# Performance work log

Hardware: AMD Instinct MI355X
Metric: run time of the kernel (lower is better)

## Reference

```python
import jax, jax.numpy as jnp
import numpy as np

CHEB_K = 2  # hops per support; stacked terms = 1 + 2*CHEB_K = 5


def setup_inputs() -> dict:
    key = jax.random.key(0)
    k1, k2, k3, k4, k5 = jax.random.split(key, 5)
    B, N, C, O, D = 16, 1024, 64, 64, 10
    return {
        "x": jax.random.normal(k1, (B, N, C), dtype=jnp.float32),
        "adj": jax.random.uniform(k2, (2, B, N, N), dtype=jnp.float32),
        "node_embedding": jax.random.normal(k3, (N, D), dtype=jnp.float32),
        "weights_pool": jax.random.normal(k4, (D, 2 * CHEB_K + 1, C, O), dtype=jnp.float32) * 0.1,
        "bias_pool": jax.random.normal(k5, (D, O), dtype=jnp.float32) * 0.1,
    }


def reference(x, adj, node_embedding, weights_pool, bias_pool):
    # k-hop graph aggregation over each of the 2 supports
    out = [x]
    for s in range(adj.shape[0]):
        a = adj[s]  # [B, N, N]
        x1 = x
        for _ in range(CHEB_K):
            x1 = jnp.einsum('bnm,bmc->bnc', a, x1)
            out.append(x1)
    x_g = jnp.stack(out, axis=2)  # [B, N, K, C] with K = 2*cheb_k+1 (already node-major)
    # per-node hypernetwork weights and bias from node embeddings
    weights = jnp.einsum('nd,dkio->nkio', node_embedding, weights_pool)  # [N, K, C, O]
    bias = node_embedding @ bias_pool  # [N, O]
    # per-node contraction over (K, C)
    return jnp.einsum('bnki,nkio->bno', x_g, weights) + bias
```

## Files before the change

### kernel.cpp

```cpp
#include <hip/hip_runtime.h>
#include <stdint.h>


typedef __attribute__((ext_vector_type(4))) float f32x4;
typedef __attribute__((ext_vector_type(2))) float f32x2;
typedef __attribute__((ext_vector_type(8))) short s16x8;
typedef __attribute__((ext_vector_type(8))) __bf16 bf16x8;

__device__ __forceinline__ unsigned short f2bf(float f) {
  union { float f; uint32_t u; } v; v.f = f;
  uint32_t r = v.u + 0x7FFFu + ((v.u >> 16) & 1u);
  return (unsigned short)(r >> 16);
}
__device__ __forceinline__ uint32_t pack2(float a, float b) {
  return (uint32_t)f2bf(a) | ((uint32_t)f2bf(b) << 16);
}

union FragU { s16x8 s; bf16x8 b; };

__device__ __forceinline__ void async_cp16(const void* g, void* l) {
  __builtin_amdgcn_global_load_lds(
      (const __attribute__((address_space(1))) void*)g,
      (__attribute__((address_space(3))) void*)l, 16, 0, 0);
}

#define WAITVM(n)                                                         \
  __builtin_amdgcn_s_waitcnt(((n) & 15) | ((((n) >> 4) & 3) << 14) |      \
                             (7 << 4) | (15 << 8))

__global__ __launch_bounds__(256) void prep(const float* __restrict__ x,
                                            const float* __restrict__ wp,
                                            unsigned short* __restrict__ XT0,
                                            float* __restrict__ wpT) {
  __shared__ __align__(16) char smem[17160];
  const int tid = threadIdx.x;
  const int bid = blockIdx.x;
  if (bid < 256) {
    unsigned short (*tl)[72] = (unsigned short(*)[72])smem;
    const int b = bid >> 4, n0 = (bid & 15) * 64;
    {
      const int c4 = (tid & 15) * 4;
#pragma unroll
      for (int i = 0; i < 4; ++i) {
        const int row = (tid >> 4) + i * 16;
        f32x4 v =
            *(const f32x4*)(x + ((size_t)(b * 1024 + n0 + row)) * 64 + c4);
        *(uint32_t*)&tl[row][c4]     = pack2(v[0], v[1]);
        *(uint32_t*)&tl[row][c4 + 2] = pack2(v[2], v[3]);
      }
    }
    __syncthreads();
    {
      const int c = tid >> 2;
      const int nch = (tid & 3) * 16;
      s16x8 s0, s1;
#pragma unroll
      for (int j = 0; j < 8; ++j) {
        s0[j] = (short)tl[nch + j][c];
        s1[j] = (short)tl[nch + 8 + j][c];
      }
      unsigned short* p = XT0 + (size_t)(b * 64 + c) * 1024 + n0 + nch;
      *(s16x8*)p = s0;
      *(s16x8*)(p + 8) = s1;
    }
  } else {
    float (*tl)[65] = (float(*)[65])smem;
    const int jj = bid - 256;
    const int d = jj / 5, ki0 = (jj % 5) * 64;
    const float* src = wp + (size_t)d * 20480;
    {
      const int o4 = (tid & 15) * 4;
#pragma unroll
      for (int i = 0; i < 4; ++i) {
        const int row = (tid >> 4) + i * 16;
        f32x4 v = *(const f32x4*)(src + (size_t)(ki0 + row) * 64 + o4);
        tl[row][o4] = v[0]; tl[row][o4 + 1] = v[1];
        tl[row][o4 + 2] = v[2]; tl[row][o4 + 3] = v[3];
      }
    }
    __syncthreads();
    {
      const int o = tid >> 2;
      const int kch = (tid & 3) * 16;
      float* dst = wpT + (size_t)d * 20480 + (size_t)o * 320 + ki0 + kch;
#pragma unroll
      for (int u = 0; u < 4; ++u) {
        f32x4 v = { tl[kch + 4 * u][o], tl[kch + 4 * u + 1][o],
                    tl[kch + 4 * u + 2][o], tl[kch + 4 * u + 3][o] };
        *(f32x4*)(dst + 4 * u) = v;
      }
    }
  }
}

__device__ __forceinline__ void hop_body(
    char* smem, const float* __restrict__ A,
    const unsigned short* __restrict__ XT, float* __restrict__ Xout,
    unsigned short* __restrict__ XTout, int write_xt, int rowbase) {
  const int tid = threadIdx.x;
  const int wave = tid >> 6, lane = tid & 63;
  const int l15 = lane & 15, q = lane >> 4;

  float* const Abase = (float*)smem + wave * 3072;

  const float* ag[4];
#pragma unroll
  for (int i = 0; i < 4; ++i) {
    const int wl = i * 4 + (lane >> 4);
    const int ch = (lane & 15) ^ (wl & 7);
    ag[i] = A + (size_t)(rowbase + wave * 16 + wl) * 1024 + ch * 4;
  }
  const unsigned short* bg[8];
#pragma unroll
  for (int t = 0; t < 4; ++t)
#pragma unroll
    for (int h = 0; h < 2; ++h)
      bg[t * 2 + h] = XT + (size_t)(t * 16 + l15) * 1024 + h * 32 + q * 8;

  f32x4 acc[4];
#pragma unroll
  for (int t = 0; t < 4; ++t) acc[t] = (f32x4){0.f, 0.f, 0.f, 0.f};

  s16x8 breg0[8], breg1[8], breg2[8];

  auto issueA = [&](int k0, int s) {
#pragma unroll
    for (int i = 0; i < 4; ++i)
      async_cp16(ag[i] + k0, Abase + s * 1024 + i * 256);
  };
  auto issueB = [&](int k0, s16x8 (&br)[8]) {
#pragma unroll
    for (int j = 0; j < 8; ++j) br[j] = *(const s16x8*)(bg[j] + k0);
  };
  auto compute = [&](int s, const s16x8 (&br)[8]) {
    const float* Ab = Abase + s * 1024;
    const int sw = l15 & 7;
#pragma unroll
    for (int h = 0; h < 2; ++h) {
      const int j0 = h * 8 + q * 2;
      f32x4 c0 = *(const f32x4*)(Ab + l15 * 64 + (j0 ^ sw) * 4);
      f32x4 c1 = *(const f32x4*)(Ab + l15 * 64 + ((j0 + 1) ^ sw) * 4);
      FragU af;
#pragma unroll
      for (int e = 0; e < 4; ++e) {
        af.s[e]     = (short)f2bf(c0[e]);
        af.s[e + 4] = (short)f2bf(c1[e]);
      }
#pragma unroll
      for (int t = 0; t < 4; ++t) {
        FragU bf; bf.s = br[t * 2 + h];
        acc[t] = __builtin_amdgcn_mfma_f32_16x16x32_bf16(af.b, bf.b, acc[t],
                                                         0, 0, 0);
      }
    }
  };

  issueA(0, 0);     issueB(0, breg0);
  issueA(64, 1);    issueB(64, breg1);
  issueA(128, 2);   issueB(128, breg2);
#pragma unroll 1
  for (int kt = 0; kt < 12; kt += 3) {
    WAITVM(24);
    compute(0, breg0);
    issueA((kt + 3) * 64, 0); issueB((kt + 3) * 64, breg0);
    WAITVM(24);
    compute(1, breg1);
    issueA((kt + 4) * 64, 1); issueB((kt + 4) * 64, breg1);
    WAITVM(24);
    compute(2, breg2);
    issueA((kt + 5) * 64, 2); issueB((kt + 5) * 64, breg2);
  }
  WAITVM(24);
  compute(0, breg0);
  issueA(960, 0); issueB(960, breg0);
  WAITVM(24);
  compute(1, breg1);
  WAITVM(12);
  compute(2, breg2);
  WAITVM(0);
  compute(0, breg0);

  __syncthreads();
  float (*tile)[65] = (float(*)[65])smem;
#pragma unroll
  for (int t = 0; t < 4; ++t)
#pragma unroll
    for (int rr = 0; rr < 4; ++rr)
      tile[wave * 16 + q * 4 + rr][t * 16 + l15] = acc[t][rr];
  __syncthreads();

  {
    const int row = tid >> 2;
    const int cb = (tid & 3) * 16;
    float* __restrict__ outp = Xout + (size_t)(rowbase + row) * 64 + cb;
#pragma unroll
    for (int u = 0; u < 4; ++u) {
      f32x4 v = { tile[row][cb + 4 * u], tile[row][cb + 4 * u + 1],
                  tile[row][cb + 4 * u + 2], tile[row][cb + 4 * u + 3] };
      *(f32x4*)(outp + 4 * u) = v;
    }
  }
  if (write_xt) {
    const int c = tid >> 2;
    const int nch = (tid & 3) * 16;
    unsigned short* __restrict__ xtp = XTout + (size_t)c * 1024 + rowbase + nch;
    s16x8 s0, s1;
#pragma unroll
    for (int j = 0; j < 8; ++j) {
      s0[j] = (short)f2bf(tile[nch + j][c]);
      s1[j] = (short)f2bf(tile[nch + 8 + j][c]);
    }
    *(s16x8*)xtp = s0;
    *(s16x8*)(xtp + 8) = s1;
  }
}

__global__ __launch_bounds__(256, 2) void hop1_kernel(
    const float* __restrict__ adj, const unsigned short* __restrict__ XT0,
    float* __restrict__ X1, unsigned short* __restrict__ XT1,
    const float* __restrict__ wpT, const float* __restrict__ emb,
    unsigned short* __restrict__ WT) {
  __shared__ __align__(16) char smem[49152];
  const int bx = blockIdx.x, slice = blockIdx.y, b = slice & 15;
  hop_body(smem, adj + (size_t)slice * 1048576, XT0 + (size_t)b * 65536,
           X1 + (size_t)slice * 65536, XT1 + (size_t)slice * 65536, 1,
           bx * 64);

  const int bid = slice * 16 + bx;
  const int tid = threadIdx.x;
#pragma unroll 1
  for (int j = bid * 5; j < bid * 5 + 5; ++j) {
    const int jx = j % 40;
    const int n0 = (j / 40) * 16;
    const int idx = (jx * 256 + tid) * 2;
    f32x2 wv[10];
#pragma unroll
    for (int d = 0; d < 10; ++d)
      wv[d] = *(const f32x2*)(wpT + (size_t)d * 20480 + idx);
#pragma unroll
    for (int g = 0; g < 16; ++g) {
      float a0 = 0.f, a1 = 0.f;
#pragma unroll
      for (int d = 0; d < 10; ++d) {
        const float e = emb[(n0 + g) * 10 + d];
        a0 += e * wv[d][0];
        a1 += e * wv[d][1];
      }
      *(uint32_t*)(WT + (size_t)(n0 + g) * 20480 + idx) = pack2(a0, a1);
    }
  }
}

__global__ __launch_bounds__(256, 2) void hop2_kernel(
    const float* __restrict__ adj, const unsigned short* __restrict__ XT1,
    float* __restrict__ X2) {
  __shared__ __align__(16) char smem[49152];
  const int bx = 15 - (int)blockIdx.x;
  const int slice = 31 - (int)blockIdx.y;
  hop_body(smem, adj + (size_t)slice * 1048576, XT1 + (size_t)slice * 65536,
           X2 + (size_t)slice * 65536, (unsigned short*)0, 0, bx * 64);
}

__global__ __launch_bounds__(256, 2) void final_kernel(
    const float* __restrict__ x, const float* __restrict__ X1,
    const float* __restrict__ X2, const unsigned short* __restrict__ WT,
    const float* __restrict__ emb, const float* __restrict__ bias_pool,
    float* __restrict__ out) {
  __shared__ unsigned short xg[2][16][328];
  const int tid = threadIdx.x;
  const int node_base = blockIdx.x * 2;

  for (int u = tid; u < 5120; u += 256) {
    const int nd = u / 2560;
    int rem = u - nd * 2560;
    const int bb = rem / 160;
    const int kiu = rem - bb * 160;
    const int ki = kiu * 2;
    const int k = ki >> 6;
    const int c = ki & 63;
    const int nn = node_base + nd;
    const float* src;
    if (k == 0) {
      src = x + ((size_t)bb * 1024 + nn) * 64 + c;
    } else {
      const float* arr = (k == 1 || k == 3) ? X1 : X2;
      const int s = (k >= 3) ? 1 : 0;
      src = arr + ((size_t)(s * 16 + bb) * 1024 + nn) * 64 + c;
    }
    f32x2 v = *(const f32x2*)src;
    *(uint32_t*)&xg[nd][bb][ki] = pack2(v[0], v[1]);
  }
  __syncthreads();

  const int wave = tid >> 6, lane = tid & 63;
  const int nd = wave >> 1, oh = wave & 1;
  const int l15 = lane & 15, q = lane >> 4;
  const int n = node_base + nd;
  f32x4 acc[2];
#pragma unroll
  for (int t = 0; t < 2; ++t) acc[t] = (f32x4){0.f, 0.f, 0.f, 0.f};

  const unsigned short* wt0 =
      WT + (size_t)n * 20480 + (size_t)l15 * 320 + q * 8;
#pragma unroll
  for (int ks = 0; ks < 10; ++ks) {
    const int k0 = ks * 32;
    FragU af;
    af.s = *(const s16x8*)&xg[nd][l15][k0 + q * 8];
#pragma unroll
    for (int tt = 0; tt < 2; ++tt) {
      const int t = oh * 2 + tt;
      FragU bf;
      bf.s = *(const s16x8*)(wt0 + (size_t)t * (16 * 320) + k0);
      acc[tt] = __builtin_amdgcn_mfma_f32_16x16x32_bf16(af.b, bf.b, acc[tt],
                                                        0, 0, 0);
    }
  }

#pragma unroll
  for (int tt = 0; tt < 2; ++tt) {
    const int o = (oh * 2 + tt) * 16 + l15;
    float bv = 0.f;
#pragma unroll
    for (int d = 0; d < 10; ++d)
      bv += emb[n * 10 + d] * bias_pool[d * 64 + o];
#pragma unroll
    for (int rr = 0; rr < 4; ++rr) {
      const int bb = q * 4 + rr;
      out[((size_t)bb * 1024 + n) * 64 + o] = acc[tt][rr] + bv;
    }
  }
}

extern "C" void kernel_launch(void* const* d_in, const int* in_sizes, int n_in,
                              void* d_out, int out_size, void* d_ws,
                              size_t ws_size, hipStream_t stream) {
  const float* x   = (const float*)d_in[0];
  const float* adj = (const float*)d_in[1];
  const float* emb = (const float*)d_in[2];
  const float* wp  = (const float*)d_in[3];
  const float* bp  = (const float*)d_in[4];
  float* out = (float*)d_out;

  char* ws = (char*)d_ws;
  unsigned short* XT0 = (unsigned short*)(ws);
  unsigned short* XT1 = (unsigned short*)(ws + ((size_t)2 << 20));
  float* X1  = (float*)(ws + ((size_t)6 << 20));
  float* X2  = (float*)(ws + ((size_t)14 << 20));
  float* wpT = (float*)(ws + ((size_t)22 << 20));
  unsigned short* WT = (unsigned short*)(ws + ((size_t)23 << 20));

  prep<<<dim3(306), dim3(256), 0, stream>>>(x, wp, XT0, wpT);
  hop1_kernel<<<dim3(16, 32), dim3(256), 0, stream>>>(adj, XT0, X1, XT1,
                                                      wpT, emb, WT);
  hop2_kernel<<<dim3(16, 32), dim3(256), 0, stream>>>(adj, XT1, X2);
  final_kernel<<<dim3(512), dim3(256), 0, stream>>>(x, X1, X2, WT, emb, bp,
                                                    out);
}
```

Measured before the change: 278.6 us.

## Pre-convert adjacency to bf16 and stage both GEMM operands through LDS

Adds a separate pass that converts the whole fp32 adjacency tensor to bf16 in workspace, so the hop kernels read half-size A tiles and drop the per-element fp32-to-bf16 conversion from the MFMA inner loop. The hop mainloop is rewritten from a three-stage register/LDS pipeline with fine-grained vmcnt waits into a two-stage LDS double buffer for both A and XT, synchronised with __syncthreads. LDS per block shrinks, so launch bounds are raised to 4 blocks per CU. The cost is an extra kernel that reads the full adjacency and writes a bf16 copy, which adds total memory traffic, plus a barrier-based pipeline that may hide latency less well.

```diff
diff --git a/kernel.cpp b/kernel.cpp
--- a/kernel.cpp
+++ b/kernel.cpp
@@ -24,9 +24,21 @@
       (__attribute__((address_space(3))) void*)l, 16, 0, 0);
 }
 
-#define WAITVM(n)                                                         \
-  __builtin_amdgcn_s_waitcnt(((n) & 15) | ((((n) >> 4) & 3) << 14) |      \
-                             (7 << 4) | (15 << 8))
+__global__ __launch_bounds__(256) void cvt_adj(const float* __restrict__ adj,
+                                               unsigned short* __restrict__ adjb) {
+  const size_t stride = (size_t)gridDim.x * 256 * 8;
+  for (size_t p = ((size_t)blockIdx.x * 256 + threadIdx.x) * 8;
+       p < 33554432u; p += stride) {
+    f32x4 a = *(const f32x4*)(adj + p);
+    f32x4 b = *(const f32x4*)(adj + p + 4);
+    union { s16x8 s; uint32_t u[4]; } o;
+    o.u[0] = pack2(a[0], a[1]);
+    o.u[1] = pack2(a[2], a[3]);
+    o.u[2] = pack2(b[0], b[1]);
+    o.u[3] = pack2(b[2], b[3]);
+    *(s16x8*)(adjb + p) = o.s;
+  }
+}
 
 __global__ __launch_bounds__(256) void prep(const float* __restrict__ x,
                                             const float* __restrict__ wp,
@@ -94,91 +106,67 @@
 }
 
 __device__ __forceinline__ void hop_body(
-    char* smem, const float* __restrict__ A,
+    char* smem, const unsigned short* __restrict__ A,
     const unsigned short* __restrict__ XT, float* __restrict__ Xout,
     unsigned short* __restrict__ XTout, int write_xt, int rowbase) {
   const int tid = threadIdx.x;
   const int wave = tid >> 6, lane = tid & 63;
   const int l15 = lane & 15, q = lane >> 4;
 
-  float* const Abase = (float*)smem + wave * 3072;
-
-  const float* ag[4];
-#pragma unroll
-  for (int i = 0; i < 4; ++i) {
-    const int wl = i * 4 + (lane >> 4);
-    const int ch = (lane & 15) ^ (wl & 7);
-    ag[i] = A + (size_t)(rowbase + wave * 16 + wl) * 1024 + ch * 4;
-  }
-  const unsigned short* bg[8];
-#pragma unroll
-  for (int t = 0; t < 4; ++t)
-#pragma unroll
-    for (int h = 0; h < 2; ++h)
-      bg[t * 2 + h] = XT + (size_t)(t * 16 + l15) * 1024 + h * 32 + q * 8;
+  unsigned short* const Ast = (unsigned short*)smem;
+  unsigned short* const Bst = (unsigned short*)smem + 8192;
+
+  const int sub = lane >> 3;
+  const int ch = lane & 7;
+  const unsigned short* asrc[2];
+  const unsigned short* bsrc[2];
+  int ldso[2];
+#pragma unroll
+  for (int i = 0; i < 2; ++i) {
+    const int r = wave * 16 + i * 8 + sub;
+    asrc[i] = A + (size_t)(rowbase + r) * 1024 + (ch ^ (r & 7)) * 8;
+    bsrc[i] = XT + (size_t)r * 1024 + (ch ^ (r & 7)) * 8;
+    ldso[i] = (wave * 16 + i * 8) * 64;
+  }
 
   f32x4 acc[4];
 #pragma unroll
   for (int t = 0; t < 4; ++t) acc[t] = (f32x4){0.f, 0.f, 0.f, 0.f};
 
-  s16x8 breg0[8], breg1[8], breg2[8];
-
-  auto issueA = [&](int k0, int s) {
-#pragma unroll
-    for (int i = 0; i < 4; ++i)
-      async_cp16(ag[i] + k0, Abase + s * 1024 + i * 256);
+  auto issue = [&](int s, int k0) {
+#pragma unroll
+    for (int i = 0; i < 2; ++i) {
+      async_cp16(asrc[i] + k0, Ast + s * 4096 + ldso[i]);
+      async_cp16(bsrc[i] + k0, Bst + s * 4096 + ldso[i]);
+    }
   };
-  auto issueB = [&](int k0, s16x8 (&br)[8]) {
-#pragma unroll
-    for (int j = 0; j < 8; ++j) br[j] = *(const s16x8*)(bg[j] + k0);
-  };
-  auto compute = [&](int s, const s16x8 (&br)[8]) {
-    const float* Ab = Abase + s * 1024;
-    const int sw = l15 & 7;
+  const int sw = l15 & 7;
+  auto compute = [&](int s) {
+    const unsigned short* Ab = Ast + s * 4096 + (wave * 16 + l15) * 64;
+    const unsigned short* Bb = Bst + s * 4096 + l15 * 64;
 #pragma unroll
     for (int h = 0; h < 2; ++h) {
-      const int j0 = h * 8 + q * 2;
-      f32x4 c0 = *(const f32x4*)(Ab + l15 * 64 + (j0 ^ sw) * 4);
-      f32x4 c1 = *(const f32x4*)(Ab + l15 * 64 + ((j0 + 1) ^ sw) * 4);
+      const int cko = ((h * 4 + q) ^ sw) * 8;
       FragU af;
-#pragma unroll
-      for (int e = 0; e < 4; ++e) {
-        af.s[e]     = (short)f2bf(c0[e]);
-        af.s[e + 4] = (short)f2bf(c1[e]);
-      }
+      af.s = *(const s16x8*)(Ab + cko);
 #pragma unroll
       for (int t = 0; t < 4; ++t) {
-        FragU bf; bf.s = br[t * 2 + h];
+        FragU bf;
+        bf.s = *(const s16x8*)(Bb + t * 1024 + cko);
         acc[t] = __builtin_amdgcn_mfma_f32_16x16x32_bf16(af.b, bf.b, acc[t],
                                                          0, 0, 0);
       }
     }
   };
 
-  issueA(0, 0);     issueB(0, breg0);
-  issueA(64, 1);    issueB(64, breg1);
-  issueA(128, 2);   issueB(128, breg2);
+  issue(0, 0);
 #pragma unroll 1
-  for (int kt = 0; kt < 12; kt += 3) {
-    WAITVM(24);
-    compute(0, breg0);
-    issueA((kt + 3) * 64, 0); issueB((kt + 3) * 64, breg0);
-    WAITVM(24);
-    compute(1, breg1);
-    issueA((kt + 4) * 64, 1); issueB((kt + 4) * 64, breg1);
-    WAITVM(24);
-    compute(2, breg2);
-    issueA((kt + 5) * 64, 2); issueB((kt + 5) * 64, breg2);
-  }
-  WAITVM(24);
-  compute(0, breg0);
-  issueA(960, 0); issueB(960, breg0);
-  WAITVM(24);
-  compute(1, breg1);
-  WAITVM(12);
-  compute(2, breg2);
-  WAITVM(0);
-  compute(0, breg0);
+  for (int kt = 0; kt < 16; ++kt) {
+    const int cur = kt & 1;
+    __syncthreads();
+    if (kt + 1 < 16) issue(cur ^ 1, (kt + 1) * 64);
+    compute(cur);
+  }
 
   __syncthreads();
   float (*tile)[65] = (float(*)[65])smem;
@@ -215,14 +203,14 @@
   }
 }
 
-__global__ __launch_bounds__(256, 2) void hop1_kernel(
-    const float* __restrict__ adj, const unsigned short* __restrict__ XT0,
-    float* __restrict__ X1, unsigned short* __restrict__ XT1,
-    const float* __restrict__ wpT, const float* __restrict__ emb,
-    unsigned short* __restrict__ WT) {
-  __shared__ __align__(16) char smem[49152];
+__global__ __launch_bounds__(256, 4) void hop1_kernel(
+    const unsigned short* __restrict__ adjb,
+    const unsigned short* __restrict__ XT0, float* __restrict__ X1,
+    unsigned short* __restrict__ XT1, const float* __restrict__ wpT,
+    const float* __restrict__ emb, unsigned short* __restrict__ WT) {
+  __shared__ __align__(16) char smem[32768];
   const int bx = blockIdx.x, slice = blockIdx.y, b = slice & 15;
-  hop_body(smem, adj + (size_t)slice * 1048576, XT0 + (size_t)b * 65536,
+  hop_body(smem, adjb + (size_t)slice * 1048576, XT0 + (size_t)b * 65536,
            X1 + (size_t)slice * 65536, XT1 + (size_t)slice * 65536, 1,
            bx * 64);
 
@@ -251,13 +239,13 @@
   }
 }
 
-__global__ __launch_bounds__(256, 2) void hop2_kernel(
-    const float* __restrict__ adj, const unsigned short* __restrict__ XT1,
-    float* __restrict__ X2) {
-  __shared__ __align__(16) char smem[49152];
+__global__ __launch_bounds__(256, 4) void hop2_kernel(
+    const unsigned short* __restrict__ adjb,
+    const unsigned short* __restrict__ XT1, float* __restrict__ X2) {
+  __shared__ __align__(16) char smem[32768];
   const int bx = 15 - (int)blockIdx.x;
   const int slice = 31 - (int)blockIdx.y;
-  hop_body(smem, adj + (size_t)slice * 1048576, XT1 + (size_t)slice * 65536,
+  hop_body(smem, adjb + (size_t)slice * 1048576, XT1 + (size_t)slice * 65536,
            X2 + (size_t)slice * 65536, (unsigned short*)0, 0, bx * 64);
 }
 
@@ -349,11 +337,13 @@
   float* X2  = (float*)(ws + ((size_t)14 << 20));
   float* wpT = (float*)(ws + ((size_t)22 << 20));
   unsigned short* WT = (unsigned short*)(ws + ((size_t)23 << 20));
-
+  unsigned short* adjb = (unsigned short*)(ws + ((size_t)64 << 20));
+
+  cvt_adj<<<dim3(8192), dim3(256), 0, stream>>>(adj, adjb);
   prep<<<dim3(306), dim3(256), 0, stream>>>(x, wp, XT0, wpT);
-  hop1_kernel<<<dim3(16, 32), dim3(256), 0, stream>>>(adj, XT0, X1, XT1,
+  hop1_kernel<<<dim3(16, 32), dim3(256), 0, stream>>>(adjb, XT0, X1, XT1,
                                                       wpT, emb, WT);
-  hop2_kernel<<<dim3(16, 32), dim3(256), 0, stream>>>(adj, XT1, X2);
+  hop2_kernel<<<dim3(16, 32), dim3(256), 0, stream>>>(adjb, XT1, X2);
   final_kernel<<<dim3(512), dim3(256), 0, stream>>>(x, X1, X2, WT, emb, bp,
                                                     out);
 }
```

After: 271.1 us. 1.03x faster.
